# Kernel tuning notes

Measured on AMD Instinct MI355X. Metric: run time of the kernel, lower is better.

The kernel has to match this reference:

```python
import jax, jax.numpy as jnp
import numpy as np


def _adj(p):
    # p: [B,N,C] -> W = exp(-pairwise squared distance), fully dense (incl. self loops)
    sq = jnp.sum(p * p, axis=-1, keepdims=True)            # [B,N,1]
    d = sq - 2.0 * jnp.einsum('bnc,bmc->bnm', p, p) + jnp.swapaxes(sq, 1, 2)
    return jnp.exp(-d)


def _cheb_lap(W):
    # PyG ChebConv norm with sym normalization, lambda_max=2: L_hat = L - I = -D^{-1/2} W D^{-1/2}
    dinv = jax.lax.rsqrt(jnp.sum(W, axis=-1))              # [B,N]
    return -(dinv[:, :, None] * W * dinv[:, None, :])


def _reg_lap(W):
    # get_laplacian(sym) after remove_self_loops: L = I - D'^{-1/2} W' D'^{-1/2}, W' = W with zero diag
    N = W.shape[1]
    eye = jnp.eye(N, dtype=W.dtype)
    W0 = W * (1.0 - eye)
    dinv = jax.lax.rsqrt(jnp.sum(W0, axis=-1))
    return eye - dinv[:, :, None] * W0 * dinv[:, None, :]


def _cheb(x, Lhat, Wk, b):
    # Chebyshev recursion: Z0=x, Z1=L_hat x, Zk = 2 L_hat Z_{k-1} - Z_{k-2}
    # x: [B,N,Cin], Lhat: [B,N,N], Wk: [K,Cin,Cout]
    Z0 = x
    out = jnp.einsum('bni,io->bno', Z0, Wk[0])
    if Wk.shape[0] > 1:
        Z1 = jnp.einsum('bnm,bmi->bni', Lhat, x)
        out = out + jnp.einsum('bni,io->bno', Z1, Wk[1])
        for k in range(2, Wk.shape[0]):
            Z2 = 2.0 * jnp.einsum('bnm,bmi->bni', Lhat, Z1) - Z0
            out = out + jnp.einsum('bni,io->bno', Z2, Wk[k])
            Z0, Z1 = Z1, Z2
    return out + b


def _reg(out, L):
    # ||out^T L out||_F, block-diagonal L -> sum over batch blocks
    M = jnp.einsum('bnc,bnm,bmd->cd', out, L, out)
    return jnp.linalg.norm(M)


def setup_inputs() -> dict:
    key = jax.random.key(0)
    ks = jax.random.split(key, 16)
    B, N = 16, 1024
    s = 0.05
    return {
        'x': jax.random.normal(ks[0], (B, N, 6), dtype=jnp.float32),
        'batch': jnp.repeat(jnp.arange(B, dtype=jnp.int64 if jax.config.jax_enable_x64 else jnp.int32), N),
        'batch_size': B,
        'nr_points': N,
        'w1': jax.random.normal(ks[1], (6, 6, 128), dtype=jnp.float32) * s,
        'b1': jnp.zeros((128,), dtype=jnp.float32),
        'w2': jax.random.normal(ks[2], (5, 128, 512), dtype=jnp.float32) * s,
        'b2': jnp.zeros((512,), dtype=jnp.float32),
        'w3': jax.random.normal(ks[3], (3, 512, 1024), dtype=jnp.float32) * s,
        'b3': jnp.zeros((1024,), dtype=jnp.float32),
        'fw1': jax.random.normal(ks[4], (1024, 512), dtype=jnp.float32) * s,
        'fb1': jnp.zeros((512,), dtype=jnp.float32),
        'fw2': jax.random.normal(ks[5], (512, 128), dtype=jnp.float32) * s,
        'fb2': jnp.zeros((128,), dtype=jnp.float32),
        'fw3': jax.random.normal(ks[6], (128, 10), dtype=jnp.float32) * s,
        'fb3': jnp.zeros((10,), dtype=jnp.float32),
    }


def reference(x, batch, batch_size, nr_points, w1, b1, w2, b2, w3, b3,
              fw1, fb1, fw2, fb2, fw3, fb3):
    sg = jax.lax.stop_gradient
    # reshape of x happens inside torch.no_grad -> input to conv1 is detached
    h = sg(x)
    W1 = sg(_adj(x))
    out = jax.nn.relu(_cheb(h, _cheb_lap(W1), w1, b1))            # [B,N,128]
    r1 = sg(_reg(out, _reg_lap(W1)))
    W2 = sg(_adj(out))
    out = jax.nn.relu(_cheb(out, sg(_cheb_lap(W2)), w2, b2))      # [B,N,512]
    r2 = sg(_reg(out, _reg_lap(W2)))
    W3 = sg(_adj(out))
    out = jax.nn.relu(_cheb(out, sg(_cheb_lap(W3)), w3, b3))      # [B,N,1024]
    r3 = sg(_reg(out, _reg_lap(W3)))
    pooled = jnp.max(out, axis=1)                                  # MaxPool1d over points
    h = jax.nn.relu(pooled @ fw1 + fb1)
    h = jax.nn.relu(h @ fw2 + fb2)
    logits = h @ fw3 + fb3
    return logits, r1, r2, r3
```

## Files before the change

### kernel.cpp

```cpp
#include <hip/hip_runtime.h>

#define BB 16
#define NN 1024
#define LDT 16384

typedef float4 f4;
typedef __attribute__((ext_vector_type(8))) short bf16x8;
typedef __attribute__((ext_vector_type(4))) float f32x4;

__device__ __forceinline__ unsigned f2b1(float f) {
    unsigned u = __builtin_bit_cast(unsigned, f);
    return (u + 0x7fffu + ((u >> 16) & 1u)) >> 16;
}
__device__ __forceinline__ float b2f1(unsigned s) {
    unsigned u = (s & 0xffffu) << 16;
    return __builtin_bit_cast(float, u);
}

#define SW(r, k) ((r) * 64 + ((k) ^ (((((r) & 7) ^ (((r) >> 3) & 7))) << 3)))

__device__ __forceinline__ void gload16(const unsigned short* g, short* l) {
    __builtin_amdgcn_global_load_lds(
        (const __attribute__((address_space(1))) unsigned int*)g,
        (__attribute__((address_space(3))) unsigned int*)l, 16, 0, 0);
}

__device__ __forceinline__ float wave_sum(float v) {
    #pragma unroll
    for (int m = 32; m >= 1; m >>= 1) v += __shfl_xor(v, m);
    return v;
}
__device__ __forceinline__ float wave_max(float v) {
    #pragma unroll
    for (int m = 32; m >= 1; m >>= 1) v = fmaxf(v, __shfl_xor(v, m));
    return v;
}

__device__ __forceinline__ void stage_tr(short* T, const unsigned short* src,
                                         size_t col_base, int c0, int Cvalid, int tid) {
    #pragma unroll
    for (int n = 0; n < 2; n++) {
        int q = n * 256 + tid;
        int p = q >> 4, h = q & 15;
        int cg = c0 + 2 * p;
        uint4 r0 = make_uint4(0, 0, 0, 0), r1 = make_uint4(0, 0, 0, 0);
        if (cg < Cvalid)     r0 = *(const uint4*)&src[(size_t)cg * LDT + col_base + 8 * h];
        if (cg + 1 < Cvalid) r1 = *(const uint4*)&src[(size_t)(cg + 1) * LDT + col_base + 8 * h];
        const unsigned* a0 = (const unsigned*)&r0;
        const unsigned* a1 = (const unsigned*)&r1;
        #pragma unroll
        for (int e = 0; e < 8; e++) {
            unsigned lo = (e & 1) ? (a0[e >> 1] >> 16) : (a0[e >> 1] & 0xffffu);
            unsigned hi = (e & 1) ? (a1[e >> 1] >> 16) : (a1[e >> 1] & 0xffffu);
            int r = 8 * h + e;
            *(unsigned*)&T[SW(r, 2 * p)] = lo | (hi << 16);
        }
    }
}

__global__ void xt_prep_kernel(const float* __restrict__ x, short* __restrict__ xh,
                               short* __restrict__ xl) {
    int m = blockIdx.x * 256 + threadIdx.x;
    #pragma unroll
    for (int c = 0; c < 8; c++) {
        float v = (c < 6) ? x[(size_t)m * 6 + c] : 0.f;
        unsigned h = f2b1(v);
        unsigned l = f2b1(v - b2f1(h));
        xh[(size_t)c * LDT + m] = (short)h;
        xl[(size_t)c * LDT + m] = (short)l;
    }
}

__global__ void wtt_prep_kernel(const float* __restrict__ Wk, short* __restrict__ WtT,
                                int Kp64, int KpValid, int CpadM1, int shift, int Cin, int Cout) {
    int idx = blockIdx.x * 256 + threadIdx.x;
    if (idx >= Cout * Kp64) return;
    int co = idx / Kp64, kk = idx - co * Kp64;
    int c = kk & CpadM1;
    float val = 0.f;
    if (kk < KpValid && c < Cin)
        val = Wk[((size_t)(kk >> shift) * Cin + c) * Cout + co];
    WtT[(size_t)co * Kp64 + kk] = (short)f2b1(val);
}

__global__ void wtrans_kernel(const float* __restrict__ Wt, float* __restrict__ WtT,
                              int K, int O) {
    int idx = blockIdx.x * 256 + threadIdx.x;
    if (idx >= K * O) return;
    int o = idx / K, k = idx - o * K;
    WtT[idx] = Wt[(size_t)k * O + o];
}

__global__ void scale_sc_kernel(const short* __restrict__ src, const float* __restrict__ coeff,
                                short* __restrict__ dst, int total8) {
    int q = blockIdx.x * 256 + threadIdx.x;
    if (q >= total8) return;
    size_t base = (size_t)q * 8;
    int m8 = (int)(base & (LDT - 1));
    uint4 v = *(const uint4*)&((const unsigned short*)src)[base];
    f4 c0 = *(const f4*)&coeff[m8];
    f4 c1 = *(const f4*)&coeff[m8 + 4];
    const float* cp0 = (const float*)&c0;
    const float* cp1 = (const float*)&c1;
    unsigned* vp = (unsigned*)&v;
    #pragma unroll
    for (int e = 0; e < 4; e++) {
        float se0 = (e < 2) ? cp0[2 * e] : cp1[2 * e - 4];
        float se1 = (e < 2) ? cp0[2 * e + 1] : cp1[2 * e - 3];
        vp[e] = f2b1(b2f1(vp[e]) * se0) | (f2b1(b2f1(vp[e] >> 16) * se1) << 16);
    }
    *(uint4*)&((unsigned short*)dst)[base] = v;
}

__global__ __launch_bounds__(256)
void xpose_kernel(const short* __restrict__ H, const short* __restrict__ L,
                  int Cvalid, int CR, short* __restrict__ XRh, short* __restrict__ XRl) {
    __shared__ short Th[128 * 64], Tl[128 * 64];
    int tid = threadIdx.x;
    int m0 = blockIdx.x * 128, c0 = blockIdx.y * 64;
    stage_tr(Th, (const unsigned short*)H, m0, c0, Cvalid, tid);
    stage_tr(Tl, (const unsigned short*)L, m0, c0, Cvalid, tid);
    __syncthreads();
    #pragma unroll
    for (int n = 0; n < 4; n++) {
        int q = n * 256 + tid;
        int r = q >> 3, j = q & 7;
        int g = (r & 7) ^ ((r >> 3) & 7);
        *(uint4*)&XRh[(size_t)(m0 + r) * CR + c0 + 8 * j] = *(const uint4*)&Th[r * 64 + 8 * (j ^ g)];
        *(uint4*)&XRl[(size_t)(m0 + r) * CR + c0 + 8 * j] = *(const uint4*)&Tl[r * 64 + 8 * (j ^ g)];
    }
}

__global__ void sqt_part_kernel(const short* __restrict__ H, const short* __restrict__ L,
                                int C, float* __restrict__ dst) {
    int m = blockIdx.x * 256 + threadIdx.x;
    int cb = blockIdx.y * 128;
    int ce = min(cb + 128, C);
    const unsigned short* Hp = (const unsigned short*)H;
    const unsigned short* Lp = (const unsigned short*)L;
    float s = 0.f;
    for (int c = cb; c < ce; c++) {
        float v = b2f1(Hp[(size_t)c * LDT + m]) + b2f1(Lp[(size_t)c * LDT + m]);
        s += v * v;
    }
    dst[(size_t)blockIdx.y * LDT + m] = s;
}
__global__ void sqt_red_kernel(const float* __restrict__ part, int NC, float* __restrict__ sq) {
    int m = blockIdx.x * 256 + threadIdx.x;
    float s = 0.f;
    for (int y = 0; y < NC; y++) s += part[(size_t)y * LDT + m];
    sq[m] = s;
}

__global__ __launch_bounds__(256)
void adj_mfma_kernel(const short* __restrict__ XRh, const short* __restrict__ XRl,
                     int ck64, int CR, const float* __restrict__ sq,
                     short* __restrict__ Wb, float* __restrict__ Wpart,
                     float* __restrict__ diagW) {
    __shared__ short Ah[128 * 64], Al[128 * 64], Bh[128 * 64], Bl[128 * 64];
    __shared__ float jpart[128][2];
    int tid = threadIdx.x, lane = tid & 63, w = tid >> 6;
    int wj = w >> 1, wi = w & 1;
    int b = blockIdx.z, i0 = blockIdx.x * 128, j0 = blockIdx.y * 128;
    size_t bo = (size_t)b * NN;
    f32x4 acc[4][4] = {};
    const unsigned short* Hp = (const unsigned short*)XRh;
    const unsigned short* Lp = (const unsigned short*)XRl;
    int rr = lane >> 3, jj = lane & 7;
    size_t offI[4], offJ[4];
    #pragma unroll
    for (int m = 0; m < 4; m++) {
        int s = w + m * 4;
        int jc = jj ^ rr ^ (s & 7);
        offI[m] = (size_t)(bo + i0 + 8 * s + rr) * CR + 8 * jc;
        offJ[m] = (size_t)(bo + j0 + 8 * s + rr) * CR + 8 * jc;
    }
    for (int t = 0; t < ck64; t++) {
        int c0 = t * 64;
        #pragma unroll
        for (int m = 0; m < 4; m++) {
            int s512 = (w + m * 4) * 512;
            gload16(Hp + offI[m] + c0, Ah + s512);
            gload16(Lp + offI[m] + c0, Al + s512);
            gload16(Hp + offJ[m] + c0, Bh + s512);
            gload16(Lp + offJ[m] + c0, Bl + s512);
        }
        __syncthreads();
        int la = lane & 15;
        #pragma unroll
        for (int ks = 0; ks < 2; ks++) {
            int kb = ks * 32 + (lane >> 4) * 8;
            bf16x8 jh[4], jl[4], ih[4], il[4];
            #pragma unroll
            for (int f = 0; f < 4; f++) {
                int jr = wj * 64 + f * 16 + la;
                jh[f] = *(const bf16x8*)&Bh[SW(jr, kb)];
                jl[f] = *(const bf16x8*)&Bl[SW(jr, kb)];
                int ir = wi * 64 + f * 16 + la;
                ih[f] = *(const bf16x8*)&Ah[SW(ir, kb)];
                il[f] = *(const bf16x8*)&Al[SW(ir, kb)];
            }
            #pragma unroll
            for (int fq = 0; fq < 4; fq++)
                #pragma unroll
                for (int fi = 0; fi < 4; fi++) {
                    acc[fq][fi] = __builtin_amdgcn_mfma_f32_16x16x32_bf16(jh[fq], ih[fi], acc[fq][fi], 0, 0, 0);
                    acc[fq][fi] = __builtin_amdgcn_mfma_f32_16x16x32_bf16(jh[fq], il[fi], acc[fq][fi], 0, 0, 0);
                    acc[fq][fi] = __builtin_amdgcn_mfma_f32_16x16x32_bf16(jl[fq], ih[fi], acc[fq][fi], 0, 0, 0);
                }
        }
        __syncthreads();
    }
    const float* sqb = sq + bo;
    unsigned short* Wout = (unsigned short*)Wb + bo * NN;
    float si_[4];
    int iloc[4];
    #pragma unroll
    for (int fi = 0; fi < 4; fi++) {
        iloc[fi] = i0 + wi * 64 + fi * 16 + (lane & 15);
        si_[fi] = sqb[iloc[fi]];
    }
    #pragma unroll
    for (int fq = 0; fq < 4; fq++) {
        int jb = j0 + wj * 64 + fq * 16 + (lane >> 4) * 4;
        #pragma unroll
        for (int r = 0; r < 4; r++) {
            int j = jb + r;
            float sj = sqb[j];
            float p = 0.f;
            #pragma unroll
            for (int fi = 0; fi < 4; fi++) {
                float val = __expf(2.f * ((const float*)&acc[fq][fi])[r] - si_[fi] - sj);
                Wout[(size_t)j * NN + iloc[fi]] = (unsigned short)f2b1(val);
                if (iloc[fi] == j) diagW[bo + j] = val;
                else p += val;
            }
            p += __shfl_xor(p, 1); p += __shfl_xor(p, 2);
            p += __shfl_xor(p, 4); p += __shfl_xor(p, 8);
            if ((lane & 15) == 0)
                jpart[wj * 64 + fq * 16 + (lane >> 4) * 4 + r][wi] = p;
        }
    }
    __syncthreads();
    if (tid < 128)
        Wpart[(size_t)blockIdx.x * (BB * NN) + bo + j0 + tid] = jpart[tid][0] + jpart[tid][1];
}

__global__ void reduce_prep_kernel(const float* __restrict__ Wpart, const float* __restrict__ diagW,
                                   float* dinv, float* dinvP, float* cA1, float* cA2, float* cAV) {
    int idx = blockIdx.x * 256 + threadIdx.x;
    float s = 0.f;
    #pragma unroll
    for (int x = 0; x < 8; x++) s += Wpart[(size_t)x * (BB * NN) + idx];
    float d = diagW[idx];
    float dv = rsqrtf(s + d);
    float dp = rsqrtf(s);
    dinv[idx] = dv; dinvP[idx] = dp;
    cA1[idx] = -dv; cA2[idx] = -2.f * dv; cAV[idx] = -dp;
}

template<bool HAS_PREV, bool SKIP_DIAG, bool WRITE_SC, int XB>
__global__ __launch_bounds__(512)
void wgemm2_kernel(const short* __restrict__ W, const short* __restrict__ Bsc,
                   const float* __restrict__ cAvec, float prevSign,
                   const short* __restrict__ PrevT, const float* __restrict__ scVec,
                   short* __restrict__ DstT, short* __restrict__ DstSc, int Cvalid) {
    __shared__ short As[XB * 64], Bs[128 * 64];
    constexpr int NFI = XB / 64;
    int tid = threadIdx.x, lane = tid & 63, w = tid >> 6;
    int wcc = w >> 2, wii = w & 3;
    int b = blockIdx.z, i0 = blockIdx.x * XB, c0 = blockIdx.y * 128;
    size_t bo = (size_t)b * NN;
    const unsigned short* Wp = (const unsigned short*)W + bo * NN;
    const unsigned short* Bp = (const unsigned short*)Bsc;
    int rr = lane >> 3, jj = lane & 7;
    int jc = jj ^ rr ^ (w & 7);
    const unsigned short* aR0 = Wp + (size_t)(i0 + 8 * w + rr) * NN + 8 * jc;
    const unsigned short* aR1 = Wp + (size_t)(i0 + 8 * ((XB == 128) ? w + 8 : w) + rr) * NN + 8 * jc;
    const unsigned short* bR0 = Bp + (size_t)(c0 + 8 * w + rr) * LDT + bo + 8 * jc;
    const unsigned short* bR1 = Bp + (size_t)(c0 + 8 * (w + 8) + rr) * LDT + bo + 8 * jc;
    short* aL0 = As + w * 512;
    short* aL1 = As + ((XB == 128) ? w + 8 : w) * 512;
    short* bL0 = Bs + w * 512; short* bL1 = Bs + (w + 8) * 512;
    f32x4 acc[4][NFI] = {};
    for (int k0 = 0; k0 < NN; k0 += 64) {
        gload16(aR0 + k0, aL0);
        if (XB == 128) gload16(aR1 + k0, aL1);
        gload16(bR0 + k0, bL0);
        gload16(bR1 + k0, bL1);
        __syncthreads();
        if (SKIP_DIAG) {
            if (k0 >= i0 && k0 < i0 + XB) {
                if (tid < 64) As[SW((k0 - i0) + tid, tid)] = 0;
                __syncthreads();
            }
        }
        int la = lane & 15;
        #pragma unroll
        for (int ks = 0; ks < 2; ks++) {
            int kb = ks * 32 + (lane >> 4) * 8;
            bf16x8 ac[4], bi[NFI];
            #pragma unroll
            for (int f = 0; f < 4; f++) ac[f] = *(const bf16x8*)&Bs[SW(wcc * 64 + f * 16 + la, kb)];
            #pragma unroll
            for (int f = 0; f < NFI; f++) bi[f] = *(const bf16x8*)&As[SW(wii * (XB / 4) + f * 16 + la, kb)];
            #pragma unroll
            for (int fq = 0; fq < 4; fq++)
                #pragma unroll
                for (int fi = 0; fi < NFI; fi++)
                    acc[fq][fi] = __builtin_amdgcn_mfma_f32_16x16x32_bf16(ac[fq], bi[fi], acc[fq][fi], 0, 0, 0);
        }
        __syncthreads();
    }
    const unsigned short* Pp = (const unsigned short*)PrevT;
    unsigned short* Dp = (unsigned short*)DstT;
    unsigned short* Sp = (unsigned short*)DstSc;
    #pragma unroll
    for (int fi = 0; fi < NFI; fi++) {
        int i = i0 + wii * (XB / 4) + fi * 16 + (lane & 15);
        float ca = cAvec[bo + i];
        float sc = WRITE_SC ? scVec[bo + i] : 0.f;
        #pragma unroll
        for (int fq = 0; fq < 4; fq++) {
            int cb = c0 + wcc * 64 + fq * 16 + (lane >> 4) * 4;
            const float* av = (const float*)&acc[fq][fi];
            #pragma unroll
            for (int r = 0; r < 4; r++) {
                int c = cb + r;
                if (c < Cvalid) {
                    float v = ca * av[r];
                    if (HAS_PREV) v += prevSign * b2f1(Pp[(size_t)c * LDT + bo + i]);
                    Dp[(size_t)c * LDT + bo + i] = (unsigned short)f2b1(v);
                    if (WRITE_SC) Sp[(size_t)c * LDT + bo + i] = (unsigned short)f2b1(v * sc);
                }
            }
        }
    }
}

__global__ __launch_bounds__(512)
void fgemm_mfma_kernel(const short* __restrict__ A0T, const short* __restrict__ ZrT,
                       const short* __restrict__ WtT, int Kp64, int KpValid, int Cpad,
                       const float* __restrict__ bias,
                       short* __restrict__ OutH, short* __restrict__ OutL) {
    __shared__ short As[128 * 64], Bs[128 * 64];
    int tid = threadIdx.x, lane = tid & 63, w = tid >> 6;
    int wco = w >> 2, wm = w & 3;
    int m0 = blockIdx.x * 128, co0 = blockIdx.y * 128;
    const unsigned short* A0 = (const unsigned short*)A0T;
    const unsigned short* Zr = (const unsigned short*)ZrT;
    const unsigned short* Wt = (const unsigned short*)WtT;
    int rr = lane >> 3, jj = lane & 7;
    int jcB = jj ^ rr ^ (w & 7);
    const unsigned short* bB0 = Wt + (size_t)(co0 + 8 * w + rr) * Kp64 + 8 * jcB;
    const unsigned short* bB1 = Wt + (size_t)(co0 + 8 * (w + 8) + rr) * Kp64 + 8 * jcB;
    short* bL0 = Bs + w * 512; short* bL1 = Bs + (w + 8) * 512;
    int p = tid >> 4, h = tid & 15;
    uint4 ra0, ra1;
    auto loadA = [&](int kk0) {
        int kg0 = kk0 + 2 * p;
        ra0 = make_uint4(0, 0, 0, 0); ra1 = make_uint4(0, 0, 0, 0);
        if (kg0 < KpValid) {
            const unsigned short* s0 = (kg0 < Cpad) ? (A0 + (size_t)kg0 * LDT)
                                                    : (Zr + (size_t)(kg0 - Cpad) * LDT);
            ra0 = *(const uint4*)&s0[m0 + 8 * h];
        }
        if (kg0 + 1 < KpValid) {
            int kg1 = kg0 + 1;
            const unsigned short* s1 = (kg1 < Cpad) ? (A0 + (size_t)kg1 * LDT)
                                                    : (Zr + (size_t)(kg1 - Cpad) * LDT);
            ra1 = *(const uint4*)&s1[m0 + 8 * h];
        }
    };
    f32x4 acc[4][2] = {};
    loadA(0);
    for (int kk0 = 0; kk0 < Kp64; kk0 += 64) {
        {
            const unsigned* a0 = (const unsigned*)&ra0;
            const unsigned* a1 = (const unsigned*)&ra1;
            #pragma unroll
            for (int e = 0; e < 8; e++) {
                unsigned lo = (e & 1) ? (a0[e >> 1] >> 16) : (a0[e >> 1] & 0xffffu);
                unsigned hi = (e & 1) ? (a1[e >> 1] >> 16) : (a1[e >> 1] & 0xffffu);
                *(unsigned*)&As[SW(8 * h + e, 2 * p)] = lo | (hi << 16);
            }
        }
        gload16(bB0 + kk0, bL0);
        gload16(bB1 + kk0, bL1);
        __syncthreads();
        if (kk0 + 64 < Kp64) loadA(kk0 + 64);
        int la = lane & 15;
        #pragma unroll
        for (int ks = 0; ks < 2; ks++) {
            int kb = ks * 32 + (lane >> 4) * 8;
            bf16x8 ac[4], bm[2];
            #pragma unroll
            for (int f = 0; f < 4; f++) ac[f] = *(const bf16x8*)&Bs[SW(wco * 64 + f * 16 + la, kb)];
            #pragma unroll
            for (int f = 0; f < 2; f++) bm[f] = *(const bf16x8*)&As[SW(wm * 32 + f * 16 + la, kb)];
            #pragma unroll
            for (int fq = 0; fq < 4; fq++)
                #pragma unroll
                for (int fi = 0; fi < 2; fi++)
                    acc[fq][fi] = __builtin_amdgcn_mfma_f32_16x16x32_bf16(ac[fq], bm[fi], acc[fq][fi], 0, 0, 0);
        }
        __syncthreads();
    }
    unsigned short* OH = (unsigned short*)OutH;
    unsigned short* OL = (unsigned short*)OutL;
    #pragma unroll
    for (int fi = 0; fi < 2; fi++) {
        int m = m0 + wm * 32 + fi * 16 + (lane & 15);
        #pragma unroll
        for (int fq = 0; fq < 4; fq++) {
            int cb = co0 + wco * 64 + fq * 16 + (lane >> 4) * 4;
            const float* av = (const float*)&acc[fq][fi];
            #pragma unroll
            for (int r = 0; r < 4; r++) {
                int co = cb + r;
                float v = av[r] + bias[co];
                v = v > 0.f ? v : 0.f;
                unsigned ph = f2b1(v);
                unsigned pl = f2b1(v - b2f1(ph));
                OH[(size_t)co * LDT + m] = (unsigned short)ph;
                OL[(size_t)co * LDT + m] = (unsigned short)pl;
            }
        }
    }
}

__global__ __launch_bounds__(256)
void mgemm_mfma_kernel(const short* __restrict__ XT, const short* __restrict__ VT,
                       float* __restrict__ Mpart, int Cout, int kChunk) {
    __shared__ short As[128 * 64], Bs[128 * 64];
    int tid = threadIdx.x, lane = tid & 63, w = tid >> 6;
    int wcj = w >> 1, wci = w & 1;
    int ci0 = blockIdx.x * 128, cj0 = blockIdx.y * 128;
    int kStart = blockIdx.z * kChunk;
    const unsigned short* Xp = (const unsigned short*)XT + (size_t)ci0 * LDT;
    const unsigned short* Vp = (const unsigned short*)VT + (size_t)cj0 * LDT;
    int rr = lane >> 3, jj = lane & 7;
    const unsigned short* aB[4];
    const unsigned short* bB[4];
    short* aL[4]; short* bL[4];
    #pragma unroll
    for (int n = 0; n < 4; n++) {
        int s = w + n * 4;
        int jc = jj ^ rr ^ (s & 7);
        aB[n] = Xp + (size_t)(8 * s + rr) * LDT + 8 * jc;
        bB[n] = Vp + (size_t)(8 * s + rr) * LDT + 8 * jc;
        aL[n] = As + s * 512; bL[n] = Bs + s * 512;
    }
    f32x4 acc[4][4] = {};
    for (int k0 = kStart; k0 < kStart + kChunk; k0 += 64) {
        #pragma unroll
        for (int n = 0; n < 4; n++) {
            gload16(aB[n] + k0, aL[n]);
            gload16(bB[n] + k0, bL[n]);
        }
        __syncthreads();
        int la = lane & 15;
        #pragma unroll
        for (int ks = 0; ks < 2; ks++) {
            int kb = ks * 32 + (lane >> 4) * 8;
            bf16x8 aj[4], bi[4];
            #pragma unroll
            for (int f = 0; f < 4; f++) {
                aj[f] = *(const bf16x8*)&Bs[SW(wcj * 64 + f * 16 + la, kb)];
                bi[f] = *(const bf16x8*)&As[SW(wci * 64 + f * 16 + la, kb)];
            }
            #pragma unroll
            for (int fq = 0; fq < 4; fq++)
                #pragma unroll
                for (int fi = 0; fi < 4; fi++)
                    acc[fq][fi] = __builtin_amdgcn_mfma_f32_16x16x32_bf16(aj[fq], bi[fi], acc[fq][fi], 0, 0, 0);
        }
        __syncthreads();
    }
    float* pt = Mpart + (size_t)blockIdx.z * Cout * Cout;
    #pragma unroll
    for (int fq = 0; fq < 4; fq++) {
        int cjb = cj0 + wcj * 64 + fq * 16 + (lane >> 4) * 4;
        #pragma unroll
        for (int fi = 0; fi < 4; fi++) {
            int ci = ci0 + wci * 64 + fi * 16 + (lane & 15);
            const float* av = (const float*)&acc[fq][fi];
            #pragma unroll
            for (int r = 0; r < 4; r++)
                pt[(size_t)(cjb + r) * Cout + ci] = av[r];
        }
    }
}

__global__ void fro1_kernel(const float* __restrict__ part, int nElem, int splitk,
                            float* __restrict__ blockSS) {
    int tid = threadIdx.x;
    float ss = 0.f;
    for (int idx = blockIdx.x * 256 + tid; idx < nElem; idx += 1024 * 256) {
        float s = 0.f;
        for (int z = 0; z < splitk; z++) s += part[(size_t)z * nElem + idx];
        ss += s * s;
    }
    __shared__ float red[256];
    red[tid] = ss; __syncthreads();
    for (int m = 128; m >= 1; m >>= 1) { if (tid < m) red[tid] += red[tid + m]; __syncthreads(); }
    if (tid == 0) blockSS[blockIdx.x] = red[0];
}
__global__ void fro2_kernel(const float* __restrict__ blockSS, float* __restrict__ outp) {
    int tid = threadIdx.x;
    float s = 0.f;
    for (int i = tid; i < 1024; i += 256) s += blockSS[i];
    __shared__ float red[256];
    red[tid] = s; __syncthreads();
    for (int m = 128; m >= 1; m >>= 1) { if (tid < m) red[tid] += red[tid + m]; __syncthreads(); }
    if (tid == 0) *outp = sqrtf(red[0]);
}

__global__ void pool_kernel(const short* __restrict__ H, const short* __restrict__ L,
                            float* __restrict__ out) {
    int wave = threadIdx.x >> 6, lane = threadIdx.x & 63;
    int r = blockIdx.x * 4 + wave;
    int co = r >> 4, b = r & 15;
    const unsigned short* h = (const unsigned short*)H + (size_t)co * LDT + b * NN;
    const unsigned short* l = (const unsigned short*)L + (size_t)co * LDT + b * NN;
    float m = -1e30f;
    #pragma unroll
    for (int it = 0; it < 2; it++) {
        int n8 = (it * 64 + lane) * 8;
        uint4 vh = *(const uint4*)&h[n8];
        uint4 vl = *(const uint4*)&l[n8];
        const unsigned* hp = (const unsigned*)&vh;
        const unsigned* lp = (const unsigned*)&vl;
        #pragma unroll
        for (int e = 0; e < 4; e++) {
            m = fmaxf(m, b2f1(hp[e]) + b2f1(lp[e]));
            m = fmaxf(m, b2f1(hp[e] >> 16) + b2f1(lp[e] >> 16));
        }
    }
    m = wave_max(m);
    if (lane == 0) out[b * 1024 + co] = m;
}

__global__ void fc_kernel(const float* __restrict__ in, const float* __restrict__ WtT,
                          const float* __restrict__ bias, float* __restrict__ out,
                          int K, int O, int doRelu) {
    int wave = threadIdx.x >> 6, lane = threadIdx.x & 63;
    int idx = blockIdx.x * 4 + wave;
    if (idx >= 16 * O) return;
    int b = idx / O, o = idx - b * O;
    const float* ib = in + (size_t)b * K;
    const float* wr = WtT + (size_t)o * K;
    float s = 0.f;
    for (int k = lane * 4; k < K; k += 256) {
        f4 a = *(const f4*)&ib[k];
        f4 wv = *(const f4*)&wr[k];
        s += a.x * wv.x + a.y * wv.y + a.z * wv.z + a.w * wv.w;
    }
    s = wave_sum(s);
    if (lane == 0) {
        s += bias[o];
        if (doRelu) s = fmaxf(s, 0.f);
        out[(size_t)b * O + o] = s;
    }
}

extern "C" void kernel_launch(void* const* d_in, const int* in_sizes, int n_in,
                              void* d_out, int out_size, void* d_ws, size_t ws_size,
                              hipStream_t stream) {
    const float* x   = (const float*)d_in[0];
    const float* w1  = (const float*)d_in[4];
    const float* b1  = (const float*)d_in[5];
    const float* w2  = (const float*)d_in[6];
    const float* b2  = (const float*)d_in[7];
    const float* w3  = (const float*)d_in[8];
    const float* b3  = (const float*)d_in[9];
    const float* fw1 = (const float*)d_in[10];
    const float* fb1 = (const float*)d_in[11];
    const float* fw2 = (const float*)d_in[12];
    const float* fb2 = (const float*)d_in[13];
    const float* fw3 = (const float*)d_in[14];
    const float* fb3 = (const float*)d_in[15];
    float* out = (float*)d_out;

    char* ws = (char*)d_ws;
    size_t off = 0;
    auto alloc = [&](size_t bytes) -> void* {
        void* p = ws + off; off += (bytes + 255) & ~(size_t)255; return p;
    };
    short* Wbuf = (short*)alloc((size_t)BB * NN * NN * 2);
    short* Zbuf = (short*)alloc((size_t)1024 * LDT * 2);
    short* ZSc  = (short*)alloc((size_t)1024 * LDT * 2);
    short* Z0Sc = (short*)alloc((size_t)512 * LDT * 2);
    short* XRh  = (short*)alloc((size_t)512 * LDT * 2);
    short* XRl  = (short*)alloc((size_t)512 * LDT * 2);
    short* o1H  = (short*)alloc((size_t)128 * LDT * 2);
    short* o1L  = (short*)alloc((size_t)128 * LDT * 2);
    short* o2H  = (short*)alloc((size_t)512 * LDT * 2);
    short* o2L  = (short*)alloc((size_t)512 * LDT * 2);
    short* o3H  = (short*)alloc((size_t)1024 * LDT * 2);
    short* o3L  = (short*)alloc((size_t)1024 * LDT * 2);
    short* xTh  = (short*)alloc((size_t)8 * LDT * 2);
    short* xTl  = (short*)alloc((size_t)8 * LDT * 2);
    short* WtT  = (short*)alloc((size_t)1024 * 1536 * 2);
    float* fwT1 = (float*)alloc((size_t)512 * 1024 * 4);
    float* fwT2 = (float*)alloc((size_t)128 * 512 * 4);
    float* fwT3 = (float*)alloc((size_t)10 * 128 * 4);
    float* sqpart = (float*)alloc((size_t)8 * LDT * 4);
    float* Wpart  = (float*)alloc((size_t)8 * BB * NN * 4);
    float* diagW  = (float*)alloc(BB * NN * 4);
    float* sq    = (float*)alloc(BB * NN * 4);
    float* dinv  = (float*)alloc(BB * NN * 4);
    float* dinvP = (float*)alloc(BB * NN * 4);
    float* cA1   = (float*)alloc(BB * NN * 4);
    float* cA2   = (float*)alloc(BB * NN * 4);
    float* cAV   = (float*)alloc(BB * NN * 4);
    float* pooled= (float*)alloc(BB * 1024 * 4);
    float* h1    = (float*)alloc(BB * 512 * 4);
    float* h2    = (float*)alloc(BB * 128 * 4);
    float* blockSS = (float*)alloc(1024 * 4);
    float* Mpart = (float*)Wbuf;
    (void)ws_size; (void)in_sizes; (void)n_in; (void)out_size;

    struct Layer {
        const short *XTh, *XTl;
        int C, K, Cpad, shift, Kp64, KpValid, Cout, splitk, rIdx;
        const float *Wk, *bk;
        short *OutH, *OutL;
    };
    Layer L[3] = {
        { xTh, xTl, 8,   6, 8,   3, 64,   48,   128,  64, 160, w1, b1, o1H, o1L },
        { o1H, o1L, 128, 5, 128, 7, 640,  640,  512,  32, 161, w2, b2, o2H, o2L },
        { o2H, o2L, 512, 3, 512, 9, 1536, 1536, 1024, 8,  162, w3, b3, o3H, o3L },
    };

    xt_prep_kernel<<<LDT / 256, 256, 0, stream>>>(x, xTh, xTl);
    wtrans_kernel<<<(1024 * 512 + 255) / 256, 256, 0, stream>>>(fw1, fwT1, 1024, 512);
    wtrans_kernel<<<(512 * 128 + 255) / 256, 256, 0, stream>>>(fw2, fwT2, 512, 128);
    wtrans_kernel<<<(128 * 10 + 255) / 256, 256, 0, stream>>>(fw3, fwT3, 128, 10);

    for (int l = 0; l < 3; l++) {
        const Layer& P = L[l];
        int NC = (P.C + 127) / 128;
        int CR = (P.Cpad < 64) ? 64 : P.Cpad;
        wtt_prep_kernel<<<(P.Cout * P.Kp64 + 255) / 256, 256, 0, stream>>>(
            P.Wk, WtT, P.Kp64, P.KpValid, P.Cpad - 1, P.shift, (l == 0) ? 6 : P.C, P.Cout);
        sqt_part_kernel<<<dim3(LDT / 256, NC), 256, 0, stream>>>(P.XTh, P.XTl, P.C, sqpart);
        sqt_red_kernel<<<LDT / 256, 256, 0, stream>>>(sqpart, NC, sq);
        xpose_kernel<<<dim3(LDT / 128, CR / 64), 256, 0, stream>>>(
            P.XTh, P.XTl, P.Cpad, CR, XRh, XRl);
        adj_mfma_kernel<<<dim3(8, 8, BB), 256, 0, stream>>>(XRh, XRl, CR / 64, CR, sq,
                                                            Wbuf, Wpart, diagW);
        reduce_prep_kernel<<<BB * NN / 256, 256, 0, stream>>>(Wpart, diagW, dinv, dinvP, cA1, cA2, cAV);

        scale_sc_kernel<<<(P.Cpad * LDT / 8 + 255) / 256, 256, 0, stream>>>(
            P.XTh, dinv, Z0Sc, P.Cpad * LDT / 8);

        int cT = (P.Cpad + 127) / 128;
        bool sm = (P.Cpad <= 128);
        auto sliceR = [&](int k) -> short* { return Zbuf + (size_t)(k - 1) * P.Cpad * LDT; };
        auto sliceS = [&](int k) -> short* { return ZSc  + (size_t)(k - 1) * P.Cpad * LDT; };
        if (P.K > 2) {
            if (sm) wgemm2_kernel<false, false, true, 64><<<dim3(NN / 64, cT, BB), 512, 0, stream>>>(
                        Wbuf, Z0Sc, cA1, 0.f, (const short*)nullptr, dinv, sliceR(1), sliceS(1), P.Cpad);
            else    wgemm2_kernel<false, false, true, 128><<<dim3(NN / 128, cT, BB), 512, 0, stream>>>(
                        Wbuf, Z0Sc, cA1, 0.f, (const short*)nullptr, dinv, sliceR(1), sliceS(1), P.Cpad);
        } else {
            if (sm) wgemm2_kernel<false, false, false, 64><<<dim3(NN / 64, cT, BB), 512, 0, stream>>>(
                        Wbuf, Z0Sc, cA1, 0.f, (const short*)nullptr, dinv, sliceR(1), (short*)nullptr, P.Cpad);
            else    wgemm2_kernel<false, false, false, 128><<<dim3(NN / 128, cT, BB), 512, 0, stream>>>(
                        Wbuf, Z0Sc, cA1, 0.f, (const short*)nullptr, dinv, sliceR(1), (short*)nullptr, P.Cpad);
        }
        for (int k = 2; k < P.K; k++) {
            const short* prevT = (k == 2) ? P.XTh : sliceR(k - 2);
            if (k < P.K - 1) {
                if (sm) wgemm2_kernel<true, false, true, 64><<<dim3(NN / 64, cT, BB), 512, 0, stream>>>(
                            Wbuf, sliceS(k - 1), cA2, -1.f, prevT, dinv, sliceR(k), sliceS(k), P.Cpad);
                else    wgemm2_kernel<true, false, true, 128><<<dim3(NN / 128, cT, BB), 512, 0, stream>>>(
                            Wbuf, sliceS(k - 1), cA2, -1.f, prevT, dinv, sliceR(k), sliceS(k), P.Cpad);
            } else {
                if (sm) wgemm2_kernel<true, false, false, 64><<<dim3(NN / 64, cT, BB), 512, 0, stream>>>(
                            Wbuf, sliceS(k - 1), cA2, -1.f, prevT, dinv, sliceR(k), (short*)nullptr, P.Cpad);
                else    wgemm2_kernel<true, false, false, 128><<<dim3(NN / 128, cT, BB), 512, 0, stream>>>(
                            Wbuf, sliceS(k - 1), cA2, -1.f, prevT, dinv, sliceR(k), (short*)nullptr, P.Cpad);
            }
        }
        fgemm_mfma_kernel<<<dim3(LDT / 128, P.Cout / 128), 512, 0, stream>>>(
            P.XTh, Zbuf, WtT, P.Kp64, P.KpValid, P.Cpad, P.bk, P.OutH, P.OutL);
        scale_sc_kernel<<<(P.Cout * LDT / 8 + 255) / 256, 256, 0, stream>>>(
            P.OutH, dinvP, ZSc, P.Cout * LDT / 8);
        int cTV = P.Cout / 128;
        if (P.Cout <= 128)
            wgemm2_kernel<true, true, false, 64><<<dim3(NN / 64, cTV, BB), 512, 0, stream>>>(
                Wbuf, ZSc, cAV, 1.f, P.OutH, dinvP, Zbuf, (short*)nullptr, P.Cout);
        else
            wgemm2_kernel<true, true, false, 128><<<dim3(NN / 128, cTV, BB), 512, 0, stream>>>(
                Wbuf, ZSc, cAV, 1.f, P.OutH, dinvP, Zbuf, (short*)nullptr, P.Cout);
        int kChunk = LDT / P.splitk;
        mgemm_mfma_kernel<<<dim3(P.Cout / 128, P.Cout / 128, P.splitk), 256, 0, stream>>>(
            P.OutH, Zbuf, Mpart, P.Cout, kChunk);
        fro1_kernel<<<1024, 256, 0, stream>>>(Mpart, P.Cout * P.Cout, P.splitk, blockSS);
        fro2_kernel<<<1, 256, 0, stream>>>(blockSS, out + P.rIdx);
    }
    pool_kernel<<<16384 / 4, 256, 0, stream>>>(o3H, o3L, pooled);
    fc_kernel<<<(16 * 512 + 3) / 4, 256, 0, stream>>>(pooled, fwT1, fb1, h1, 1024, 512, 1);
    fc_kernel<<<(16 * 128 + 3) / 4, 256, 0, stream>>>(h1, fwT2, fb2, h2, 512, 128, 1);
    fc_kernel<<<(16 * 10 + 3) / 4, 256, 0, stream>>>(h2, fwT3, fb3, out, 128, 10, 0);
}
```

Baseline: 920.0 us.

## Double-buffer LDS tiles in wgemm2 and fgemm kernels to overlap loads with MFMA

Both GEMM kernels now hold two LDS buffers per operand. Each iteration issues the next tile's global-to-LDS loads (and register prefetch plus unpack for fgemm's A) into the alternate buffer while computing on the current one, with one barrier per iteration instead of two. The goal is to hide global memory latency behind MFMA work. The cost is doubled shared memory per block, which may reduce occupancy. There is also a possible hazard: the SKIP_DIAG path zeroes the current tile and syncs while async loads into the other buffer are still outstanding.

After: 897.1 us. 1.03x faster.

```diff
diff --git a/kernel.cpp b/kernel.cpp
--- a/kernel.cpp
+++ b/kernel.cpp
@@ -265,7 +265,7 @@
                    const float* __restrict__ cAvec, float prevSign,
                    const short* __restrict__ PrevT, const float* __restrict__ scVec,
                    short* __restrict__ DstT, short* __restrict__ DstSc, int Cvalid) {
-    __shared__ short As[XB * 64], Bs[128 * 64];
+    __shared__ short As[2][XB * 64], Bs[2][128 * 64];
     constexpr int NFI = XB / 64;
     int tid = threadIdx.x, lane = tid & 63, w = tid >> 6;
     int wcc = w >> 2, wii = w & 3;
@@ -279,19 +279,26 @@
     const unsigned short* aR1 = Wp + (size_t)(i0 + 8 * ((XB == 128) ? w + 8 : w) + rr) * NN + 8 * jc;
     const unsigned short* bR0 = Bp + (size_t)(c0 + 8 * w + rr) * LDT + bo + 8 * jc;
     const unsigned short* bR1 = Bp + (size_t)(c0 + 8 * (w + 8) + rr) * LDT + bo + 8 * jc;
-    short* aL0 = As + w * 512;
-    short* aL1 = As + ((XB == 128) ? w + 8 : w) * 512;
-    short* bL0 = Bs + w * 512; short* bL1 = Bs + (w + 8) * 512;
+    int aO0 = w * 512;
+    int aO1 = ((XB == 128) ? w + 8 : w) * 512;
+    int bO0 = w * 512, bO1 = (w + 8) * 512;
+    auto STAGE = [&](int k0, int buf) {
+        gload16(aR0 + k0, As[buf] + aO0);
+        if (XB == 128) gload16(aR1 + k0, As[buf] + aO1);
+        gload16(bR0 + k0, Bs[buf] + bO0);
+        gload16(bR1 + k0, Bs[buf] + bO1);
+    };
     f32x4 acc[4][NFI] = {};
-    for (int k0 = 0; k0 < NN; k0 += 64) {
-        gload16(aR0 + k0, aL0);
-        if (XB == 128) gload16(aR1 + k0, aL1);
-        gload16(bR0 + k0, bL0);
-        gload16(bR1 + k0, bL1);
-        __syncthreads();
+    STAGE(0, 0);
+    __syncthreads();
+    int cur = 0;
+    for (int t = 0; t < NN / 64; t++) {
+        int k0 = t * 64;
+        bool more = (t + 1 < NN / 64);
+        if (more) STAGE(k0 + 64, cur ^ 1);
         if (SKIP_DIAG) {
             if (k0 >= i0 && k0 < i0 + XB) {
-                if (tid < 64) As[SW((k0 - i0) + tid, tid)] = 0;
+                if (tid < 64) As[cur][SW((k0 - i0) + tid, tid)] = 0;
                 __syncthreads();
             }
         }
@@ -301,16 +308,17 @@
             int kb = ks * 32 + (lane >> 4) * 8;
             bf16x8 ac[4], bi[NFI];
             #pragma unroll
-            for (int f = 0; f < 4; f++) ac[f] = *(const bf16x8*)&Bs[SW(wcc * 64 + f * 16 + la, kb)];
-            #pragma unroll
-            for (int f = 0; f < NFI; f++) bi[f] = *(const bf16x8*)&As[SW(wii * (XB / 4) + f * 16 + la, kb)];
+            for (int f = 0; f < 4; f++) ac[f] = *(const bf16x8*)&Bs[cur][SW(wcc * 64 + f * 16 + la, kb)];
+            #pragma unroll
+            for (int f = 0; f < NFI; f++) bi[f] = *(const bf16x8*)&As[cur][SW(wii * (XB / 4) + f * 16 + la, kb)];
             #pragma unroll
             for (int fq = 0; fq < 4; fq++)
                 #pragma unroll
                 for (int fi = 0; fi < NFI; fi++)
                     acc[fq][fi] = __builtin_amdgcn_mfma_f32_16x16x32_bf16(ac[fq], bi[fi], acc[fq][fi], 0, 0, 0);
         }
-        __syncthreads();
+        if (more) __syncthreads();
+        cur ^= 1;
     }
     const unsigned short* Pp = (const unsigned short*)PrevT;
     unsigned short* Dp = (unsigned short*)DstT;
@@ -343,7 +351,7 @@
                        const short* __restrict__ WtT, int Kp64, int KpValid, int Cpad,
                        const float* __restrict__ bias,
                        short* __restrict__ OutH, short* __restrict__ OutL) {
-    __shared__ short As[128 * 64], Bs[128 * 64];
+    __shared__ short As[2][128 * 64], Bs[2][128 * 64];
     int tid = threadIdx.x, lane = tid & 63, w = tid >> 6;
     int wco = w >> 2, wm = w & 3;
     int m0 = blockIdx.x * 128, co0 = blockIdx.y * 128;
@@ -354,7 +362,7 @@
     int jcB = jj ^ rr ^ (w & 7);
     const unsigned short* bB0 = Wt + (size_t)(co0 + 8 * w + rr) * Kp64 + 8 * jcB;
     const unsigned short* bB1 = Wt + (size_t)(co0 + 8 * (w + 8) + rr) * Kp64 + 8 * jcB;
-    short* bL0 = Bs + w * 512; short* bL1 = Bs + (w + 8) * 512;
+    int bO0 = w * 512, bO1 = (w + 8) * 512;
     int p = tid >> 4, h = tid & 15;
     uint4 ra0, ra1;
     auto loadA = [&](int kk0) {
@@ -372,39 +380,50 @@
             ra1 = *(const uint4*)&s1[m0 + 8 * h];
         }
     };
+    auto unpackA = [&](int buf) {
+        const unsigned* a0 = (const unsigned*)&ra0;
+        const unsigned* a1 = (const unsigned*)&ra1;
+        #pragma unroll
+        for (int e = 0; e < 8; e++) {
+            unsigned lo = (e & 1) ? (a0[e >> 1] >> 16) : (a0[e >> 1] & 0xffffu);
+            unsigned hi = (e & 1) ? (a1[e >> 1] >> 16) : (a1[e >> 1] & 0xffffu);
+            *(unsigned*)&As[buf][SW(8 * h + e, 2 * p)] = lo | (hi << 16);
+        }
+    };
     f32x4 acc[4][2] = {};
     loadA(0);
+    gload16(bB0, Bs[0] + bO0);
+    gload16(bB1, Bs[0] + bO1);
+    unpackA(0);
+    __syncthreads();
+    int cur = 0;
     for (int kk0 = 0; kk0 < Kp64; kk0 += 64) {
-        {
-            const unsigned* a0 = (const unsigned*)&ra0;
-            const unsigned* a1 = (const unsigned*)&ra1;
-            #pragma unroll
-            for (int e = 0; e < 8; e++) {
-                unsigned lo = (e & 1) ? (a0[e >> 1] >> 16) : (a0[e >> 1] & 0xffffu);
-                unsigned hi = (e & 1) ? (a1[e >> 1] >> 16) : (a1[e >> 1] & 0xffffu);
-                *(unsigned*)&As[SW(8 * h + e, 2 * p)] = lo | (hi << 16);
-            }
-        }
-        gload16(bB0 + kk0, bL0);
-        gload16(bB1 + kk0, bL1);
-        __syncthreads();
-        if (kk0 + 64 < Kp64) loadA(kk0 + 64);
+        bool more = (kk0 + 64 < Kp64);
+        if (more) {
+            loadA(kk0 + 64);
+            gload16(bB0 + kk0 + 64, Bs[cur ^ 1] + bO0);
+            gload16(bB1 + kk0 + 64, Bs[cur ^ 1] + bO1);
+        }
         int la = lane & 15;
         #pragma unroll
         for (int ks = 0; ks < 2; ks++) {
             int kb = ks * 32 + (lane >> 4) * 8;
             bf16x8 ac[4], bm[2];
             #pragma unroll
-            for (int f = 0; f < 4; f++) ac[f] = *(const bf16x8*)&Bs[SW(wco * 64 + f * 16 + la, kb)];
-            #pragma unroll
-            for (int f = 0; f < 2; f++) bm[f] = *(const bf16x8*)&As[SW(wm * 32 + f * 16 + la, kb)];
+            for (int f = 0; f < 4; f++) ac[f] = *(const bf16x8*)&Bs[cur][SW(wco * 64 + f * 16 + la, kb)];
+            #pragma unroll
+            for (int f = 0; f < 2; f++) bm[f] = *(const bf16x8*)&As[cur][SW(wm * 32 + f * 16 + la, kb)];
             #pragma unroll
             for (int fq = 0; fq < 4; fq++)
                 #pragma unroll
                 for (int fi = 0; fi < 2; fi++)
                     acc[fq][fi] = __builtin_amdgcn_mfma_f32_16x16x32_bf16(ac[fq], bm[fi], acc[fq][fi], 0, 0, 0);
         }
-        __syncthreads();
+        if (more) {
+            unpackA(cur ^ 1);
+            __syncthreads();
+        }
+        cur ^= 1;
     }
     unsigned short* OH = (unsigned short*)OutH;
     unsigned short* OL = (unsigned short*)OutL;
```
